# Kernel optimization log

Measured on AMD Instinct MI355X. Metric: run time of the kernel, lower is better.

Reference implementation:

```python
import jax, jax.numpy as jnp
import numpy as np

D = 768      # activation_dim
F = 16384    # dict_size
K = 64       # top-k
B = 4096     # batch of activation vectors


def setup_inputs() -> dict:
    key = jax.random.key(0)
    k1, k2, k3 = jax.random.split(key, 3)
    x = jax.random.normal(k1, (B, D), dtype=jnp.float32)
    W_enc = jax.random.normal(k2, (F, D), dtype=jnp.float32) * 0.02
    b_enc = jnp.zeros((F,), dtype=jnp.float32)
    W_dec = jax.random.normal(k3, (D, F), dtype=jnp.float32)
    # decoder columns normalized to unit norm (set_decoder_norm_to_unit_norm)
    eps = jnp.finfo(jnp.float32).eps
    W_dec = W_dec / (jnp.linalg.norm(W_dec, axis=0, keepdims=True) + eps)
    b_dec = jnp.zeros((D,), dtype=jnp.float32)
    return {"x": x, "W_enc": W_enc, "b_enc": b_enc, "W_dec": W_dec, "b_dec": b_dec}


def reference(x, W_enc, b_enc, W_dec, b_dec):
    # encode: pre_activation_BF = encoder(x - b_dec)
    pre_BF = jnp.einsum('bd,fd->bf', x - b_dec, W_enc) + b_enc
    # top-k selection along feature dim
    vals_BK, idx_BK = jax.lax.top_k(pre_BF, K)
    # scatter top-k values into sparse code buffer [B, F]
    rows = jnp.arange(pre_BF.shape[0])[:, None]
    f_BF = jnp.zeros_like(pre_BF).at[rows, idx_BK].set(vals_BK)
    # decode: x_hat = decoder(f) + b_dec
    x_hat_BD = jnp.einsum('bf,df->bd', f_BF, W_dec) + b_dec
    return x_hat_BD
```

## Files before the change

### kernel.cpp

```cpp
#include <hip/hip_runtime.h>
#include <cstdint>
#include <cstddef>

#define Dd 768
#define Ff 16384
#define Bb 4096
#define Kk 64
#define NCAND 128
#define BINS 512
#define MARGIN 0.04f

typedef __bf16 bf16x8 __attribute__((ext_vector_type(8)));
typedef float  f32x4  __attribute__((ext_vector_type(4)));
typedef unsigned short u16x8 __attribute__((ext_vector_type(8)));

__device__ __forceinline__ unsigned short f2bf(float f) {
    union { float f; unsigned u; } a; a.f = f;
    unsigned r = a.u + 0x7fffu + ((a.u >> 16) & 1u);
    return (unsigned short)(r >> 16);
}
__device__ __forceinline__ float bf2f(unsigned short h) {
    union { float f; unsigned u; } a; a.u = ((unsigned)h) << 16;
    return a.f;
}
__device__ __forceinline__ float f_lo(unsigned u) {
    union { float f; unsigned u; } a; a.u = u << 16; return a.f;
}
__device__ __forceinline__ float f_hi(unsigned u) {
    union { float f; unsigned u; } a; a.u = u & 0xffff0000u; return a.f;
}

#define GLDS16(g, l) __builtin_amdgcn_global_load_lds( \
    (const __attribute__((address_space(1))) void*)(g), \
    (__attribute__((address_space(3))) void*)(l), 16, 0, 0)

__global__ __launch_bounds__(256) void conv_x(
    const float* __restrict__ x, const float* __restrict__ bdec,
    unsigned short* __restrict__ Xb)
{
    const int i = blockIdx.x * 256 + threadIdx.x;
    const int col = i % Dd;
    Xb[i] = f2bf(x[i] - bdec[col]);
}

__global__ __launch_bounds__(256) void conv_w(
    const float* __restrict__ Wenc, unsigned short* __restrict__ Wb)
{
    const int i = blockIdx.x * 256 + threadIdx.x;
    Wb[i] = f2bf(Wenc[i]);
}

__global__ __launch_bounds__(512, 2) void sae_gemm(
    const unsigned short* __restrict__ Xb,
    const unsigned short* __restrict__ Wb,
    const float* __restrict__ benc,
    unsigned short* __restrict__ pre)
{
    __shared__ __align__(128) unsigned short As[32768];
    __shared__ __align__(128) unsigned short Bs[32768];

    const int tid  = threadIdx.x;
    const int lane = tid & 63;
    const int w    = tid >> 6;
    const int wm   = w >> 2, wn = w & 3;

    const int bid = blockIdx.x;
    const int xcd = bid & 7;
    const int c   = bid >> 3;
    const int n0  = (xcd * 8 + (c & 7)) * 256;
    const int m0  = (c >> 3) * 256;

    const int r0 = tid >> 2,           r1 = (512 + tid) >> 2;
    const int q0 = (tid - (tid >> 3)) & 3;
    const int q1 = ((512 + tid) - ((512 + tid) >> 3)) & 3;
    const unsigned short* aS0 = Xb + (size_t)(m0 + r0) * Dd + q0 * 8;
    const unsigned short* aS1 = Xb + (size_t)(m0 + r1) * Dd + q1 * 8;
    const unsigned short* bS0 = Wb + (size_t)(n0 + r0) * Dd + q0 * 8;
    const unsigned short* bS1 = Wb + (size_t)(n0 + r1) * Dd + q1 * 8;
    unsigned short* lA = As + w * 512;
    unsigned short* lB = Bs + w * 512;

    const int rl  = lane & 15;
    const int rot = ((lane >> 4) + (rl >> 1)) & 3;
    const unsigned asO = (unsigned)(unsigned long long)
        (__attribute__((address_space(3))) unsigned short*)&As[0];
    const unsigned bsO = (unsigned)(unsigned long long)
        (__attribute__((address_space(3))) unsigned short*)&Bs[0];
    const unsigned aRd = asO + (unsigned)((wm * 128 + rl) * 64 + rot * 16);
    const unsigned bRd = bsO + (unsigned)((wn * 64 + rl) * 64 + rot * 16);

    f32x4 acc[8][4];
    #pragma unroll
    for (int i = 0; i < 8; ++i)
        #pragma unroll
        for (int j = 0; j < 4; ++j) acc[i][j] = 0;

#define DSR(D, A) asm volatile("ds_read_b128 %0, %1" : "=v"(D) : "v"(A))
#define STG(TILE, BUF) {                                                      \
    GLDS16(aS0 + (TILE) * 32, lA + (BUF) * 8192);                             \
    GLDS16(aS1 + (TILE) * 32, lA + (BUF) * 8192 + 4096);                      \
    GLDS16(bS0 + (TILE) * 32, lB + (BUF) * 8192);                             \
    GLDS16(bS1 + (TILE) * 32, lB + (BUF) * 8192 + 4096); }
#define VM12 asm volatile("s_waitcnt vmcnt(12)" ::: "memory")
#define VM8  asm volatile("s_waitcnt vmcnt(8)"  ::: "memory")
#define VM4  asm volatile("s_waitcnt vmcnt(4)"  ::: "memory")
#define VM0  asm volatile("s_waitcnt vmcnt(0)"  ::: "memory")
#define BAR  __builtin_amdgcn_s_barrier()

#define MF1(AF, ACCH, MI, NI) acc[(ACCH)*4+(MI)][(NI)] =                      \
    __builtin_amdgcn_mfma_f32_16x16x32_bf16(                                  \
        __builtin_bit_cast(bf16x8, bfr[(NI)]),                                \
        __builtin_bit_cast(bf16x8, AF[(MI)]), acc[(ACCH)*4+(MI)][(NI)], 0, 0, 0)
#define MFQ(AF, ACCH)                                                         \
    MF1(AF,ACCH,0,0); MF1(AF,ACCH,0,1); MF1(AF,ACCH,0,2); MF1(AF,ACCH,0,3);   \
    MF1(AF,ACCH,1,0); MF1(AF,ACCH,1,1); MF1(AF,ACCH,1,2); MF1(AF,ACCH,1,3);   \
    MF1(AF,ACCH,2,0); MF1(AF,ACCH,2,1); MF1(AF,ACCH,2,2); MF1(AF,ACCH,2,3);   \
    MF1(AF,ACCH,3,0); MF1(AF,ACCH,3,1); MF1(AF,ACCH,3,2); MF1(AF,ACCH,3,3)

#define TILE(BUF, STG_STMT, VM_STMT) {                                        \
    f32x4 af0[4], af1[4], bfr[4];                                             \
    const unsigned ab = aRd + (BUF) * 16384;                                  \
    const unsigned bb = bRd + (BUF) * 16384;                                  \
    DSR(af0[0], ab);          DSR(af0[1], ab + 1024);                         \
    DSR(af0[2], ab + 2048);   DSR(af0[3], ab + 3072);                         \
    DSR(bfr[0], bb);          DSR(bfr[1], bb + 1024);                         \
    DSR(bfr[2], bb + 2048);   DSR(bfr[3], bb + 3072);                         \
    DSR(af1[0], ab + 4096);   DSR(af1[1], ab + 5120);                         \
    DSR(af1[2], ab + 6144);   DSR(af1[3], ab + 7168);                         \
    asm volatile("s_waitcnt lgkmcnt(0)" ::: "memory");                        \
    __builtin_amdgcn_sched_barrier(0);                                        \
    BAR;                                                                      \
    STG_STMT;                                                                 \
    __builtin_amdgcn_s_setprio(1);                                            \
    MFQ(af0, 0);                                                              \
    MFQ(af1, 1);                                                              \
    __builtin_amdgcn_s_setprio(0);                                            \
    VM_STMT;                                                                  \
    BAR; }

    STG(0, 0); STG(1, 1); STG(2, 2); STG(3, 3);
    VM12; BAR;

    for (int i = 0; i < 5; ++i) {
        const int tb = 4 * i + 4;
        TILE(0, STG(tb + 0, 0), VM12);
        TILE(1, STG(tb + 1, 1), VM12);
        TILE(2, STG(tb + 2, 2), VM12);
        TILE(3, STG(tb + 3, 3), VM12);
    }
    TILE(0, (void)0, VM8);
    TILE(1, (void)0, VM4);
    TILE(2, (void)0, VM0);
    TILE(3, (void)0, (void)0);

    const int rl2  = lane & 15;
    const int cg   = (lane >> 4) * 4;
    const int colb = n0 + wn * 64;
    float4 bia[4];
    #pragma unroll
    for (int ni = 0; ni < 4; ++ni)
        bia[ni] = *(const float4*)&benc[colb + ni * 16 + cg];
    #pragma unroll
    for (int mi = 0; mi < 8; ++mi) {
        const int row = m0 + wm * 128 + mi * 16 + rl2;
        unsigned short* prow = pre + (size_t)row * Ff + colb;
        #pragma unroll
        for (int ni = 0; ni < 4; ++ni) {
            const f32x4 a = acc[mi][ni];
            uint2 pk;
            pk.x = (unsigned)f2bf(a[0] + bia[ni].x)
                 | ((unsigned)f2bf(a[1] + bia[ni].y) << 16);
            pk.y = (unsigned)f2bf(a[2] + bia[ni].z)
                 | ((unsigned)f2bf(a[3] + bia[ni].w) << 16);
            *(uint2*)(prow + ni * 16 + cg) = pk;
        }
    }

#undef DSR
#undef STG
#undef VM12
#undef VM8
#undef VM4
#undef VM0
#undef BAR
#undef MF1
#undef MFQ
#undef TILE
}

__global__ __launch_bounds__(256) void sae_select(
    const unsigned short* __restrict__ pre,
    int* __restrict__ ci, int* __restrict__ ccount)
{
    __shared__ unsigned hist[2][BINS];
    __shared__ float tauS[2];
    __shared__ int lcnt[2];

    const int tid = threadIdx.x;
    const int r   = tid >> 7;
    const int l   = tid & 127;
    const int rg  = blockIdx.x * 2 + r;

    for (int i = tid; i < 2 * BINS; i += 256) ((unsigned*)hist)[i] = 0;
    if (tid < 2) lcnt[tid] = 0;
    __syncthreads();

    const u16x8* rp = (const u16x8*)(pre + (size_t)rg * Ff);
    for (int j = 0; j < 16; ++j) {
        const u16x8 v8 = rp[j * 128 + l];
        #pragma unroll
        for (int c = 0; c < 8; ++c) {
            const float v = bf2f(v8[c]);
            if (v >= 1.0f) {
                const int b = min((int)(v * 128.0f), BINS - 1);
                atomicAdd(&hist[r][b], 1u);
            }
        }
    }
    __syncthreads();

    if (l == 0) {
        unsigned acc = 0; float tv = 1.0f;
        for (int j = BINS - 1; j >= 128; --j) {
            acc += hist[r][j];
            if (acc >= (unsigned)Kk) { tv = (float)j * 0.0078125f; break; }
        }
        tauS[r] = tv;
    }
    __syncthreads();

    const float thr = tauS[r] - MARGIN;
    for (int j = 0; j < 16; ++j) {
        const u16x8 v8 = rp[j * 128 + l];
        #pragma unroll
        for (int c = 0; c < 8; ++c) {
            const float v = bf2f(v8[c]);
            if (v >= thr) {
                const int p = atomicAdd(&lcnt[r], 1);
                if (p < NCAND) ci[(size_t)rg * NCAND + p] = j * 1024 + l * 8 + c;
            }
        }
    }
    __syncthreads();
    if (l == 0) ccount[rg] = min(lcnt[r], NCAND);
}

__global__ __launch_bounds__(256) void sae_rescore(
    const float* __restrict__ x, const float* __restrict__ Wenc,
    const float* __restrict__ benc, const float* __restrict__ bdec,
    const int* __restrict__ ci, const int* __restrict__ ccount,
    float* __restrict__ ovals, int* __restrict__ oidx)
{
    __shared__ float  xr[Dd];
    __shared__ int    cis[NCAND];
    __shared__ double es[NCAND];
    __shared__ int    cnt;

    const int r = blockIdx.x, tid = threadIdx.x;
    const int lane = tid & 63, w = tid >> 6;

    xr[tid]       = x[(size_t)r * Dd + tid]       - bdec[tid];
    xr[tid + 256] = x[(size_t)r * Dd + tid + 256] - bdec[tid + 256];
    xr[tid + 512] = x[(size_t)r * Dd + tid + 512] - bdec[tid + 512];
    if (tid == 0) cnt = ccount[r];
    if (tid < NCAND) cis[tid] = ci[(size_t)r * NCAND + tid];
    if (tid < Kk) { ovals[(size_t)r * Kk + tid] = 0.0f; oidx[(size_t)r * Kk + tid] = 0; }
    __syncthreads();

    for (int c = w; c < NCAND; c += 4) {
        double e = -1.0e300;
        if (c < cnt) {
            const int f = cis[c];
            const float* wrow = Wenc + (size_t)f * Dd;
            double a = 0.0;
            #pragma unroll
            for (int j = 0; j < Dd / 64; ++j)
                a = fma((double)wrow[j * 64 + lane], (double)xr[j * 64 + lane], a);
            #pragma unroll
            for (int off = 32; off > 0; off >>= 1)
                a += __shfl_xor(a, off);
            e = a + (double)benc[f];
        }
        if (lane == 0) es[c] = e;
    }
    __syncthreads();

    if (tid < NCAND) {
        const double e = es[tid];
        int rk = 0;
        for (int j = 0; j < NCAND; ++j) {
            const double ej = es[j];
            rk += (ej > e) || (ej == e && j < tid);
        }
        if (tid < cnt && rk < Kk) {
            ovals[(size_t)r * Kk + rk] = (float)e;
            oidx [(size_t)r * Kk + rk] = cis[tid];
        }
    }
}

__global__ __launch_bounds__(256) void sae_transpose(
    const float* __restrict__ Wd, unsigned short* __restrict__ WdT)
{
    __shared__ float tile[32][33];
    const int f0 = blockIdx.x * 32;
    const int d0 = blockIdx.y * 32;
    const int tx = threadIdx.x, ty = threadIdx.y;
    #pragma unroll
    for (int k = 0; k < 4; ++k)
        tile[ty + 8 * k][tx] = Wd[(size_t)(d0 + ty + 8 * k) * Ff + f0 + tx];
    __syncthreads();
    #pragma unroll
    for (int k = 0; k < 4; ++k)
        WdT[(size_t)(f0 + ty + 8 * k) * Dd + d0 + tx] = f2bf(tile[tx][ty + 8 * k]);
}

__global__ __launch_bounds__(192) void sae_decode(
    const unsigned short* __restrict__ WdT, const float* __restrict__ vals,
    const int* __restrict__ idx, const float* __restrict__ bdec,
    float* __restrict__ out)
{
    __shared__ float sv[Kk];
    __shared__ int   si[Kk];
    const int b = blockIdx.x, tid = threadIdx.x;
    if (tid < Kk) { sv[tid] = vals[(size_t)b * Kk + tid]; si[tid] = idx[(size_t)b * Kk + tid]; }
    __syncthreads();
    const int d0 = tid * 4;
    float a0 = bdec[d0], a1 = bdec[d0 + 1], a2 = bdec[d0 + 2], a3 = bdec[d0 + 3];
    for (int k = 0; k < Kk; ++k) {
        const float v = sv[k];
        const uint2 p = *(const uint2*)(WdT + (size_t)si[k] * Dd + d0);
        a0 = fmaf(v, f_lo(p.x), a0);
        a1 = fmaf(v, f_hi(p.x), a1);
        a2 = fmaf(v, f_lo(p.y), a2);
        a3 = fmaf(v, f_hi(p.y), a3);
    }
    float4 o4 = make_float4(a0, a1, a2, a3);
    *(float4*)(out + (size_t)b * Dd + d0) = o4;
}

extern "C" void kernel_launch(void* const* d_in, const int* in_sizes, int n_in,
                              void* d_out, int out_size, void* d_ws, size_t ws_size,
                              hipStream_t stream) {
    const float* x    = (const float*)d_in[0];
    const float* Wenc = (const float*)d_in[1];
    const float* benc = (const float*)d_in[2];
    const float* Wdec = (const float*)d_in[3];
    const float* bdec = (const float*)d_in[4];
    float* out = (float*)d_out;

    char* ws = (char*)d_ws;
    size_t o = 0;
    unsigned short* pre  = (unsigned short*)(ws + o); o += (size_t)Bb * Ff * 2;
    unsigned short* Xb   = (unsigned short*)(ws + o); o += (size_t)Bb * Dd * 2;
    unsigned short* Wb   = (unsigned short*)(ws + o); o += (size_t)Ff * Dd * 2;
    unsigned short* WdT  = (unsigned short*)(ws + o); o += (size_t)Ff * Dd * 2;
    int*            cib  = (int*)(ws + o);            o += (size_t)Bb * NCAND * 4;
    int*            ccnt = (int*)(ws + o);            o += (size_t)Bb * 4;
    float*          vals = (float*)(ws + o);          o += (size_t)Bb * Kk * 4;
    int*            idxb = (int*)(ws + o);

    conv_x<<<(Bb * Dd) / 256, 256, 0, stream>>>(x, bdec, Xb);
    conv_w<<<(Ff * Dd) / 256, 256, 0, stream>>>(Wenc, Wb);
    sae_gemm<<<(Bb / 256) * (Ff / 256), 512, 0, stream>>>(Xb, Wb, benc, pre);
    sae_select<<<Bb / 2, 256, 0, stream>>>(pre, cib, ccnt);
    sae_rescore<<<Bb, 256, 0, stream>>>(x, Wenc, benc, bdec, cib, ccnt, vals, idxb);
    sae_transpose<<<dim3(Ff / 32, Dd / 32), dim3(32, 8), 0, stream>>>(Wdec, WdT);
    sae_decode<<<Bb, 192, 0, stream>>>(WdT, vals, idxb, bdec, out);
}
```

Baseline: 561.3 us.

## Software-pipeline LDS fragment reads against MFMA via double-buffered registers

Restructures the encoder GEMM main loop so the LDS fragment reads for the next k-tile are issued before the MFMAs of the current tile, using two register sets (pa/qa) that alternate, with one barrier per slot instead of two. Global-to-LDS staging addressing is simplified by deriving the second row pointer from the first. The select kernel's histogram threshold is also widened from values at or above 1.0 down to 0.0, with a fallback threshold when fewer than K values are found. The extra fragment registers raise register pressure, and the wider histogram adds more atomics per row.

```diff
diff --git a/kernel.cpp b/kernel.cpp
--- a/kernel.cpp
+++ b/kernel.cpp
@@ -70,13 +70,10 @@
     const int n0  = (xcd * 8 + (c & 7)) * 256;
     const int m0  = (c >> 3) * 256;
 
-    const int r0 = tid >> 2,           r1 = (512 + tid) >> 2;
+    const int r0 = tid >> 2;
     const int q0 = (tid - (tid >> 3)) & 3;
-    const int q1 = ((512 + tid) - ((512 + tid) >> 3)) & 3;
     const unsigned short* aS0 = Xb + (size_t)(m0 + r0) * Dd + q0 * 8;
-    const unsigned short* aS1 = Xb + (size_t)(m0 + r1) * Dd + q1 * 8;
     const unsigned short* bS0 = Wb + (size_t)(n0 + r0) * Dd + q0 * 8;
-    const unsigned short* bS1 = Wb + (size_t)(n0 + r1) * Dd + q1 * 8;
     unsigned short* lA = As + w * 512;
     unsigned short* lB = Bs + w * 512;
 
@@ -95,63 +92,77 @@
         #pragma unroll
         for (int j = 0; j < 4; ++j) acc[i][j] = 0;
 
+    f32x4 pa0[4], pa1[4], pb[4];
+    f32x4 qa0[4], qa1[4], qb[4];
+
 #define DSR(D, A) asm volatile("ds_read_b128 %0, %1" : "=v"(D) : "v"(A))
 #define STG(TILE, BUF) {                                                      \
-    GLDS16(aS0 + (TILE) * 32, lA + (BUF) * 8192);                             \
-    GLDS16(aS1 + (TILE) * 32, lA + (BUF) * 8192 + 4096);                      \
-    GLDS16(bS0 + (TILE) * 32, lB + (BUF) * 8192);                             \
-    GLDS16(bS1 + (TILE) * 32, lB + (BUF) * 8192 + 4096); }
-#define VM12 asm volatile("s_waitcnt vmcnt(12)" ::: "memory")
+    GLDS16(aS0 + (TILE) * 32,            lA + (BUF) * 8192);                  \
+    GLDS16(aS0 + 128 * Dd + (TILE) * 32, lA + (BUF) * 8192 + 4096);           \
+    GLDS16(bS0 + (TILE) * 32,            lB + (BUF) * 8192);                  \
+    GLDS16(bS0 + 128 * Dd + (TILE) * 32, lB + (BUF) * 8192 + 4096); }
 #define VM8  asm volatile("s_waitcnt vmcnt(8)"  ::: "memory")
 #define VM4  asm volatile("s_waitcnt vmcnt(4)"  ::: "memory")
 #define VM0  asm volatile("s_waitcnt vmcnt(0)"  ::: "memory")
 #define BAR  __builtin_amdgcn_s_barrier()
 
-#define MF1(AF, ACCH, MI, NI) acc[(ACCH)*4+(MI)][(NI)] =                      \
+#define MF1(AF, BF, ACCH, MI, NI) acc[(ACCH)*4+(MI)][(NI)] =                  \
     __builtin_amdgcn_mfma_f32_16x16x32_bf16(                                  \
-        __builtin_bit_cast(bf16x8, bfr[(NI)]),                                \
+        __builtin_bit_cast(bf16x8, BF[(NI)]),                                 \
         __builtin_bit_cast(bf16x8, AF[(MI)]), acc[(ACCH)*4+(MI)][(NI)], 0, 0, 0)
-#define MFQ(AF, ACCH)                                                         \
-    MF1(AF,ACCH,0,0); MF1(AF,ACCH,0,1); MF1(AF,ACCH,0,2); MF1(AF,ACCH,0,3);   \
-    MF1(AF,ACCH,1,0); MF1(AF,ACCH,1,1); MF1(AF,ACCH,1,2); MF1(AF,ACCH,1,3);   \
-    MF1(AF,ACCH,2,0); MF1(AF,ACCH,2,1); MF1(AF,ACCH,2,2); MF1(AF,ACCH,2,3);   \
-    MF1(AF,ACCH,3,0); MF1(AF,ACCH,3,1); MF1(AF,ACCH,3,2); MF1(AF,ACCH,3,3)
-
-#define TILE(BUF, STG_STMT, VM_STMT) {                                        \
-    f32x4 af0[4], af1[4], bfr[4];                                             \
+#define MFQ(AF, BF, ACCH)                                                     \
+    MF1(AF,BF,ACCH,0,0); MF1(AF,BF,ACCH,0,1); MF1(AF,BF,ACCH,0,2);            \
+    MF1(AF,BF,ACCH,0,3); MF1(AF,BF,ACCH,1,0); MF1(AF,BF,ACCH,1,1);            \
+    MF1(AF,BF,ACCH,1,2); MF1(AF,BF,ACCH,1,3); MF1(AF,BF,ACCH,2,0);            \
+    MF1(AF,BF,ACCH,2,1); MF1(AF,BF,ACCH,2,2); MF1(AF,BF,ACCH,2,3);            \
+    MF1(AF,BF,ACCH,3,0); MF1(AF,BF,ACCH,3,1); MF1(AF,BF,ACCH,3,2);            \
+    MF1(AF,BF,ACCH,3,3)
+
+#define RD12(A0, A1, B, BUF) {                                                \
     const unsigned ab = aRd + (BUF) * 16384;                                  \
     const unsigned bb = bRd + (BUF) * 16384;                                  \
-    DSR(af0[0], ab);          DSR(af0[1], ab + 1024);                         \
-    DSR(af0[2], ab + 2048);   DSR(af0[3], ab + 3072);                         \
-    DSR(bfr[0], bb);          DSR(bfr[1], bb + 1024);                         \
-    DSR(bfr[2], bb + 2048);   DSR(bfr[3], bb + 3072);                         \
-    DSR(af1[0], ab + 4096);   DSR(af1[1], ab + 5120);                         \
-    DSR(af1[2], ab + 6144);   DSR(af1[3], ab + 7168);                         \
+    DSR(A0[0], ab);          DSR(A0[1], ab + 1024);                           \
+    DSR(A0[2], ab + 2048);   DSR(A0[3], ab + 3072);                           \
+    DSR(B[0], bb);           DSR(B[1], bb + 1024);                            \
+    DSR(B[2], bb + 2048);    DSR(B[3], bb + 3072);                            \
+    DSR(A1[0], ab + 4096);   DSR(A1[1], ab + 5120);                           \
+    DSR(A1[2], ab + 6144);   DSR(A1[3], ab + 7168); }
+
+#define SLOT(CA0, CA1, CB, NA0, NA1, NB, RDBUF, STG_STMT, VM_STMT) {          \
+    RD12(NA0, NA1, NB, RDBUF);                                                \
+    STG_STMT;                                                                 \
+    __builtin_amdgcn_sched_barrier(0);                                        \
+    __builtin_amdgcn_s_setprio(1);                                            \
+    MFQ(CA0, CB, 0);                                                          \
+    MFQ(CA1, CB, 1);                                                          \
+    __builtin_amdgcn_s_setprio(0);                                            \
     asm volatile("s_waitcnt lgkmcnt(0)" ::: "memory");                        \
     __builtin_amdgcn_sched_barrier(0);                                        \
-    BAR;                                                                      \
-    STG_STMT;                                                                 \
-    __builtin_amdgcn_s_setprio(1);                                            \
-    MFQ(af0, 0);                                                              \
-    MFQ(af1, 1);                                                              \
-    __builtin_amdgcn_s_setprio(0);                                            \
     VM_STMT;                                                                  \
     BAR; }
 
     STG(0, 0); STG(1, 1); STG(2, 2); STG(3, 3);
-    VM12; BAR;
+    VM8;
+    BAR;
+    RD12(pa0, pa1, pb, 0);
+    asm volatile("s_waitcnt lgkmcnt(0)" ::: "memory");
+    __builtin_amdgcn_sched_barrier(0);
+    BAR;
 
     for (int i = 0; i < 5; ++i) {
         const int tb = 4 * i + 4;
-        TILE(0, STG(tb + 0, 0), VM12);
-        TILE(1, STG(tb + 1, 1), VM12);
-        TILE(2, STG(tb + 2, 2), VM12);
-        TILE(3, STG(tb + 3, 3), VM12);
-    }
-    TILE(0, (void)0, VM8);
-    TILE(1, (void)0, VM4);
-    TILE(2, (void)0, VM0);
-    TILE(3, (void)0, (void)0);
+        SLOT(pa0, pa1, pb, qa0, qa1, qb, 1, STG(tb + 0, 0), VM8);
+        SLOT(qa0, qa1, qb, pa0, pa1, pb, 2, STG(tb + 1, 1), VM8);
+        SLOT(pa0, pa1, pb, qa0, qa1, qb, 3, STG(tb + 2, 2), VM8);
+        SLOT(qa0, qa1, qb, pa0, pa1, pb, 0, STG(tb + 3, 3), VM8);
+    }
+    SLOT(pa0, pa1, pb, qa0, qa1, qb, 1, (void)0, VM4);
+    SLOT(qa0, qa1, qb, pa0, pa1, pb, 2, (void)0, VM0);
+    SLOT(pa0, pa1, pb, qa0, qa1, qb, 3, (void)0, (void)0);
+    __builtin_amdgcn_s_setprio(1);
+    MFQ(qa0, qb, 0);
+    MFQ(qa1, qb, 1);
+    __builtin_amdgcn_s_setprio(0);
 
     const int rl2  = lane & 15;
     const int cg   = (lane >> 4) * 4;
@@ -178,14 +189,14 @@
 
 #undef DSR
 #undef STG
-#undef VM12
 #undef VM8
 #undef VM4
 #undef VM0
 #undef BAR
 #undef MF1
 #undef MFQ
-#undef TILE
+#undef RD12
+#undef SLOT
 }
 
 __global__ __launch_bounds__(256) void sae_select(
@@ -211,7 +222,7 @@
         #pragma unroll
         for (int c = 0; c < 8; ++c) {
             const float v = bf2f(v8[c]);
-            if (v >= 1.0f) {
+            if (v >= 0.0f) {
                 const int b = min((int)(v * 128.0f), BINS - 1);
                 atomicAdd(&hist[r][b], 1u);
             }
@@ -220,8 +231,8 @@
     __syncthreads();
 
     if (l == 0) {
-        unsigned acc = 0; float tv = 1.0f;
-        for (int j = BINS - 1; j >= 128; --j) {
+        unsigned acc = 0; float tv = -1.0e30f;
+        for (int j = BINS - 1; j >= 0; --j) {
             acc += hist[r][j];
             if (acc >= (unsigned)Kk) { tv = (float)j * 0.0078125f; break; }
         }
```

Result: slower. 618.5 us (+10.2%).
